# Kernel tuning notes

Measured on AMD Instinct MI355X. Metric: run time of the kernel, lower is better.

## Reference

```python
import jax, jax.numpy as jnp
import numpy as np

B, C = 512, 1000          # batch, classes
T, P = 64, 500_000        # num param tensors, elements per tensor
NW = 9                    # loss weights per tensor


def setup_inputs() -> dict:
    key = jax.random.key(0)
    k1, k2, k3, k4, k5 = jax.random.split(key, 5)
    return {
        "outputs": jax.random.normal(k1, (B, C), dtype=jnp.float32),
        "targets": jax.random.randint(k2, (B,), 0, C),
        "params": jax.random.normal(k3, (T, P), dtype=jnp.float32),
        "pretrained_params": jax.random.normal(k4, (T, P), dtype=jnp.float32),
        "loss_weights": jax.random.normal(k5, (T, NW), dtype=jnp.float32),
    }


def reference(outputs, targets, params, pretrained_params, loss_weights):
    b, c = outputs.shape
    logp = jax.nn.log_softmax(outputs, axis=1)                      # [B,C]
    probs = jnp.exp(logp)

    # cross entropy (mean over batch)
    ce = -jnp.take_along_axis(logp, targets[:, None], axis=1).mean()

    # multi-class hinge (MultiMarginLoss-style, margin=1, mean over batch, /C)
    correct = jnp.take_along_axis(outputs, targets[:, None], axis=1)  # [B,1]
    margins = jnp.maximum(0.0, 1.0 - correct + outputs)               # [B,C]
    not_correct = 1.0 - jax.nn.one_hot(targets, c, dtype=outputs.dtype)
    hinge = (margins * not_correct).sum(axis=1).mean() / c

    # KL(log_softmax(outputs) || uniform), batchmean reduction:
    # sum(u * (log u - logp)) / B
    u = 1.0 / c
    kl = (u * (jnp.log(jnp.asarray(u, outputs.dtype)) - logp)).sum() / b

    # entropy of the softmax distribution (mean over batch)
    entropy = -(probs * logp).sum(axis=1).mean()

    # global L2 norm of logits
    energy = jnp.sqrt((outputs * outputs).sum())

    # per-parameter-tensor norms (params are detached in the original)
    p = jax.lax.stop_gradient(params)
    q = jax.lax.stop_gradient(pretrained_params)
    l1_zero = jnp.abs(p).sum(axis=1)                       # [T]
    l2_zero = jnp.sqrt((p * p).sum(axis=1))                # [T]
    d = p - q
    l1_pre = jnp.abs(d).sum(axis=1)                        # [T]
    l2_pre = jnp.sqrt((d * d).sum(axis=1))                 # [T]

    t = p.shape[0]
    glob = jnp.stack([ce, hinge, kl, entropy, energy])     # [5]
    combined = jnp.concatenate(
        [jnp.broadcast_to(glob, (t, 5)),
         jnp.stack([l1_zero, l2_zero, l1_pre, l2_pre], axis=1)],
        axis=1,
    )                                                      # [T,9]

    total = (jax.nn.sigmoid(loss_weights) * combined).sum()
    return total / (t * 9)
```

## Files before the change

kernel.cpp:

```cpp
#include <hip/hip_runtime.h>
#include <hip/hip_bf16.h>
#include <math.h>

#define BB 512
#define CC 1000
#define TT 64
#define PSZ 500000
#define NW 9

#define BPT 10
#define PBLKS (TT * BPT)
#define C4 12500
#define TAIL4 212

#define WS_FLOATS (8 + TT * 4)

typedef float f32x4 __attribute__((ext_vector_type(4)));

__device__ __forceinline__ f32x4 ntload(const f32x4* a) {
    return __builtin_nontemporal_load(a);
}

__device__ __forceinline__ float block_reduce_sum(float v, float* scratch) {
    __syncthreads();
    for (int o = 32; o > 0; o >>= 1) v += __shfl_down(v, o);
    const int wave = threadIdx.x >> 6;
    if ((threadIdx.x & 63) == 0) scratch[wave] = v;
    __syncthreads();
    return scratch[0] + scratch[1] + scratch[2] + scratch[3];
}

__device__ __forceinline__ float block_reduce_max(float v, float* scratch) {
    __syncthreads();
    for (int o = 32; o > 0; o >>= 1) v = fmaxf(v, __shfl_down(v, o));
    const int wave = threadIdx.x >> 6;
    if ((threadIdx.x & 63) == 0) scratch[wave] = v;
    __syncthreads();
    return fmaxf(fmaxf(scratch[0], scratch[1]), fmaxf(scratch[2], scratch[3]));
}

__device__ __forceinline__ void acc4(const f32x4 a, const f32x4 c,
                                     float& l1z, float& s2z,
                                     float& l1p, float& s2p) {
    l1z += fabsf(a.x) + fabsf(a.y) + fabsf(a.z) + fabsf(a.w);
    s2z += a.x * a.x + a.y * a.y + a.z * a.z + a.w * a.w;
    const float dx = a.x - c.x, dy = a.y - c.y, dz = a.z - c.z, dw = a.w - c.w;
    l1p += fabsf(dx) + fabsf(dy) + fabsf(dz) + fabsf(dw);
    s2p += dx * dx + dy * dy + dz * dz + dw * dw;
}

__global__ __launch_bounds__(256, 2) void fused_kernel(
        const float* __restrict__ p, const float* __restrict__ q,
        const float* __restrict__ outlog, const int* __restrict__ tgt,
        float* __restrict__ ws) {
    __shared__ float row[CC];
    __shared__ float scratch[4];

    const int bid = blockIdx.x;
    const int tid = (int)threadIdx.x;
    if (bid < PBLKS) {
        const int t = bid / BPT;
        const f32x4* __restrict__ pb = (const f32x4*)p + (long long)bid * C4;
        const f32x4* __restrict__ qb = (const f32x4*)q + (long long)bid * C4;

        float l1z = 0.f, s2z = 0.f, l1p = 0.f, s2p = 0.f;

        #pragma unroll 1
        for (int j = 0; j < 3; ++j) {
            const f32x4* bp = pb + j * 4096 + tid;
            const f32x4* bq = qb + j * 4096 + tid;
            f32x4 A[16];
            #pragma unroll
            for (int k = 0; k < 16; ++k) A[k] = ntload(bp + k * 256);
            #pragma unroll
            for (int g = 0; g < 4; ++g) {
                f32x4 Cg[4];
                #pragma unroll
                for (int k = 0; k < 4; ++k) Cg[k] = ntload(bq + (g * 4 + k) * 256);
                #pragma unroll
                for (int k = 0; k < 4; ++k)
                    acc4(A[g * 4 + k], Cg[k], l1z, s2z, l1p, s2p);
            }
        }
        if (tid < TAIL4) {
            const f32x4 a = ntload(pb + 3 * 4096 + tid);
            const f32x4 c = ntload(qb + 3 * 4096 + tid);
            acc4(a, c, l1z, s2z, l1p, s2p);
        }

        for (int o = 32; o > 0; o >>= 1) {
            l1z += __shfl_down(l1z, o);
            s2z += __shfl_down(s2z, o);
            l1p += __shfl_down(l1p, o);
            s2p += __shfl_down(s2p, o);
        }
        if ((tid & 63) == 0) {
            float* base = ws + 8 + t * 4;
            atomicAdd(base + 0, l1z);
            atomicAdd(base + 1, s2z);
            atomicAdd(base + 2, l1p);
            atomicAdd(base + 3, s2p);
        }
    } else {
        const int b = bid - PBLKS;
        const float* __restrict__ o = outlog + (long long)b * CC;

        float sq = 0.f;
        for (int j = tid; j < CC; j += 256) {
            const float v = o[j];
            row[j] = v;
            sq += v * v;
        }
        __syncthreads();

        float m = -3.402823466e+38f;
        for (int j = tid; j < CC; j += 256) m = fmaxf(m, row[j]);
        m = block_reduce_max(m, scratch);

        float se = 0.f;
        for (int j = tid; j < CC; j += 256) se += __expf(row[j] - m);
        se = block_reduce_sum(se, scratch);
        const float logZ = m + __logf(se);

        const int tg = tgt[b];
        const float ot = row[tg];

        float ent = 0.f, lps = 0.f, hin = 0.f;
        for (int j = tid; j < CC; j += 256) {
            const float lp = row[j] - logZ;
            ent += __expf(lp) * lp;
            lps += lp;
            const float mg = 1.f - ot + row[j];
            if (j != tg && mg > 0.f) hin += mg;
        }
        sq  = block_reduce_sum(sq, scratch);
        ent = block_reduce_sum(ent, scratch);
        lps = block_reduce_sum(lps, scratch);
        hin = block_reduce_sum(hin, scratch);

        if (tid == 0) {
            atomicAdd(&ws[0], -(ot - logZ));
            atomicAdd(&ws[1], hin);
            atomicAdd(&ws[2], lps);
            atomicAdd(&ws[3], ent);
            atomicAdd(&ws[4], sq);
        }
    }
}

__global__ __launch_bounds__(256) void final_kernel(
        const float* __restrict__ lw, const float* __restrict__ ws,
        float* __restrict__ out) {
    __shared__ float scratch[4];
    const float ce      = ws[0] / (float)BB;
    const float hinge   = ws[1] / ((float)BB * (float)CC);
    const float kl      = -logf((float)CC) - ws[2] / ((float)BB * (float)CC);
    const float entropy = -ws[3] / (float)BB;
    const float energy  = sqrtf(ws[4]);
    const float glob[5] = {ce, hinge, kl, entropy, energy};

    float acc = 0.f;
    for (int i = threadIdx.x; i < TT * NW; i += 256) {
        const int t = i / NW;
        const int k = i - t * NW;
        float cmb;
        if (k < 5)       cmb = glob[k];
        else if (k == 5) cmb = ws[8 + t * 4 + 0];
        else if (k == 6) cmb = sqrtf(ws[8 + t * 4 + 1]);
        else if (k == 7) cmb = ws[8 + t * 4 + 2];
        else             cmb = sqrtf(ws[8 + t * 4 + 3]);
        const float w = 1.f / (1.f + expf(-lw[i]));
        acc += w * cmb;
    }
    acc = block_reduce_sum(acc, scratch);
    if (threadIdx.x == 0) out[0] = acc / (float)(TT * NW);
}

extern "C" void kernel_launch(void* const* d_in, const int* in_sizes, int n_in,
                              void* d_out, int out_size, void* d_ws, size_t ws_size,
                              hipStream_t stream) {
    const float* outputs    = (const float*)d_in[0];
    const int*   targets    = (const int*)d_in[1];
    const float* params     = (const float*)d_in[2];
    const float* pretrained = (const float*)d_in[3];
    const float* lw         = (const float*)d_in[4];
    float* ws  = (float*)d_ws;
    float* out = (float*)d_out;

    hipMemsetAsync(ws, 0, WS_FLOATS * sizeof(float), stream);

    fused_kernel<<<PBLKS + BB, 256, 0, stream>>>(params, pretrained, outputs, targets, ws);
    final_kernel<<<1, 256, 0, stream>>>(lw, ws, out);
}
```

Measured before the change: 77.75 us.

## Use persistent blocks with atomic work-stealing over finer param chunks

Replaces the static one-block-per-slice grid with 1024 persistent blocks. The first 512 blocks handle logit rows first, then every block pulls 25k-element parameter chunks from a global atomic counter kept in the workspace until all 1280 chunks are done. This halves the chunk size and balances load between the short logit work and the bandwidth-bound norm reduction, reducing tail imbalance. It adds an atomic and two barriers per chunk, and relies on the memset-zeroed counter slot.

```diff
diff --git a/kernel.cpp b/kernel.cpp
--- a/kernel.cpp
+++ b/kernel.cpp
@@ -8,12 +8,12 @@
 #define PSZ 500000
 #define NW 9
 
-#define BPT 10
-#define PBLKS (TT * BPT)
-#define C4 12500
-#define TAIL4 212
+#define NCHUNK 1280
+#define CPT 20
+#define CH4 6250
 
 #define WS_FLOATS (8 + TT * 4)
+#define CTR_IDX 6
 
 typedef float f32x4 __attribute__((ext_vector_type(4)));
 
@@ -49,60 +49,81 @@
     s2p += dx * dx + dy * dy + dz * dz + dw * dw;
 }
 
+__device__ __forceinline__ void do_chunk(int c, const float* __restrict__ p,
+                                         const float* __restrict__ q,
+                                         float* __restrict__ ws, int tid) {
+    const int t = c / CPT;
+    const f32x4* __restrict__ pb = (const f32x4*)p + (long long)c * CH4;
+    const f32x4* __restrict__ qb = (const f32x4*)q + (long long)c * CH4;
+
+    float l1z = 0.f, s2z = 0.f, l1p = 0.f, s2p = 0.f;
+
+    {
+        const f32x4* bp = pb + tid;
+        const f32x4* bq = qb + tid;
+        f32x4 A[16];
+        #pragma unroll
+        for (int k = 0; k < 16; ++k) A[k] = ntload(bp + k * 256);
+        #pragma unroll
+        for (int g = 0; g < 4; ++g) {
+            f32x4 Cg[4];
+            #pragma unroll
+            for (int k = 0; k < 4; ++k) Cg[k] = ntload(bq + (g * 4 + k) * 256);
+            #pragma unroll
+            for (int k = 0; k < 4; ++k)
+                acc4(A[g * 4 + k], Cg[k], l1z, s2z, l1p, s2p);
+        }
+    }
+    {
+        const f32x4* bp = pb + 4096 + tid;
+        const f32x4* bq = qb + 4096 + tid;
+        f32x4 A[8];
+        #pragma unroll
+        for (int k = 0; k < 8; ++k) A[k] = ntload(bp + k * 256);
+        #pragma unroll
+        for (int g = 0; g < 2; ++g) {
+            f32x4 Cg[4];
+            #pragma unroll
+            for (int k = 0; k < 4; ++k) Cg[k] = ntload(bq + (g * 4 + k) * 256);
+            #pragma unroll
+            for (int k = 0; k < 4; ++k)
+                acc4(A[g * 4 + k], Cg[k], l1z, s2z, l1p, s2p);
+        }
+    }
+    if (tid < CH4 - 6144) {
+        const f32x4 a = ntload(pb + 6144 + tid);
+        const f32x4 c2 = ntload(qb + 6144 + tid);
+        acc4(a, c2, l1z, s2z, l1p, s2p);
+    }
+
+    for (int o = 32; o > 0; o >>= 1) {
+        l1z += __shfl_down(l1z, o);
+        s2z += __shfl_down(s2z, o);
+        l1p += __shfl_down(l1p, o);
+        s2p += __shfl_down(s2p, o);
+    }
+    if ((tid & 63) == 0) {
+        float* base = ws + 8 + t * 4;
+        atomicAdd(base + 0, l1z);
+        atomicAdd(base + 1, s2z);
+        atomicAdd(base + 2, l1p);
+        atomicAdd(base + 3, s2p);
+    }
+}
+
 __global__ __launch_bounds__(256, 2) void fused_kernel(
         const float* __restrict__ p, const float* __restrict__ q,
         const float* __restrict__ outlog, const int* __restrict__ tgt,
         float* __restrict__ ws) {
     __shared__ float row[CC];
     __shared__ float scratch[4];
+    __shared__ int sc;
 
     const int bid = blockIdx.x;
     const int tid = (int)threadIdx.x;
-    if (bid < PBLKS) {
-        const int t = bid / BPT;
-        const f32x4* __restrict__ pb = (const f32x4*)p + (long long)bid * C4;
-        const f32x4* __restrict__ qb = (const f32x4*)q + (long long)bid * C4;
-
-        float l1z = 0.f, s2z = 0.f, l1p = 0.f, s2p = 0.f;
-
-        #pragma unroll 1
-        for (int j = 0; j < 3; ++j) {
-            const f32x4* bp = pb + j * 4096 + tid;
-            const f32x4* bq = qb + j * 4096 + tid;
-            f32x4 A[16];
-            #pragma unroll
-            for (int k = 0; k < 16; ++k) A[k] = ntload(bp + k * 256);
-            #pragma unroll
-            for (int g = 0; g < 4; ++g) {
-                f32x4 Cg[4];
-                #pragma unroll
-                for (int k = 0; k < 4; ++k) Cg[k] = ntload(bq + (g * 4 + k) * 256);
-                #pragma unroll
-                for (int k = 0; k < 4; ++k)
-                    acc4(A[g * 4 + k], Cg[k], l1z, s2z, l1p, s2p);
-            }
-        }
-        if (tid < TAIL4) {
-            const f32x4 a = ntload(pb + 3 * 4096 + tid);
-            const f32x4 c = ntload(qb + 3 * 4096 + tid);
-            acc4(a, c, l1z, s2z, l1p, s2p);
-        }
-
-        for (int o = 32; o > 0; o >>= 1) {
-            l1z += __shfl_down(l1z, o);
-            s2z += __shfl_down(s2z, o);
-            l1p += __shfl_down(l1p, o);
-            s2p += __shfl_down(s2p, o);
-        }
-        if ((tid & 63) == 0) {
-            float* base = ws + 8 + t * 4;
-            atomicAdd(base + 0, l1z);
-            atomicAdd(base + 1, s2z);
-            atomicAdd(base + 2, l1p);
-            atomicAdd(base + 3, s2p);
-        }
-    } else {
-        const int b = bid - PBLKS;
+
+    if (bid < BB) {
+        const int b = bid;
         const float* __restrict__ o = outlog + (long long)b * CC;
 
         float sq = 0.f;
@@ -145,6 +166,16 @@
             atomicAdd(&ws[3], ent);
             atomicAdd(&ws[4], sq);
         }
+    }
+
+    unsigned int* ctr = (unsigned int*)ws + CTR_IDX;
+    for (;;) {
+        if (tid == 0) sc = (int)atomicAdd(ctr, 1u);
+        __syncthreads();
+        const int c = sc;
+        __syncthreads();
+        if (c >= NCHUNK) break;
+        do_chunk(c, p, q, ws, tid);
     }
 }
 
@@ -189,6 +220,6 @@
 
     hipMemsetAsync(ws, 0, WS_FLOATS * sizeof(float), stream);
 
-    fused_kernel<<<PBLKS + BB, 256, 0, stream>>>(params, pretrained, outputs, targets, ws);
+    fused_kernel<<<1024, 256, 0, stream>>>(params, pretrained, outputs, targets, ws);
     final_kernel<<<1, 256, 0, stream>>>(lw, ws, out);
 }
```

Measured after the change: 149.0 us. +91.7%, slower.
